# Kernel tuning notes

Hardware: AMD Instinct MI355X
Metric: run time of the kernel (lower is better)

The kernel has to match this reference:

```python
import jax, jax.numpy as jnp
import numpy as np

WINDOW_SIZE = 2
SOFTMAX_TEMP = 0.01
WIDTH = 320
EPS = 1e-12  # F.normalize default eps


def _l2norm(x, axis):
    n = jnp.sqrt(jnp.sum(x * x, axis=axis, keepdims=True))
    return x / jnp.maximum(n, EPS)


def setup_inputs() -> dict:
    key = jax.random.key(0)
    k1, k2, k3, k4 = jax.random.split(key, 4)
    BW, C, N, S = 4, 256, 1024, 1
    return {
        "keypoint_scores": jax.random.uniform(k1, (BW, S, N), dtype=jnp.float32),
        "keypoint_desc": jax.random.normal(k2, (BW, C, N), dtype=jnp.float32),
        "desc_dense": jax.random.normal(k3, (BW, C, WIDTH, WIDTH), dtype=jnp.float32),
        "keypoint_coords": jax.random.uniform(k4, (BW, N, 2), dtype=jnp.float32),
    }


def reference(keypoint_scores, keypoint_desc, desc_dense, keypoint_coords):
    BW, C, N = keypoint_desc.shape
    B = BW // WINDOW_SIZE
    P = B * (WINDOW_SIZE - 1)  # number of (src, tgt) pairs

    # dense source pixel coordinates (u=col, v=row), matching torch meshgrid 'ij'
    idx = jnp.arange(WIDTH * WIDTH)
    coords = jnp.stack([(idx % WIDTH).astype(jnp.float32),
                        (idx // WIDTH).astype(jnp.float32)], axis=1)  # (HW, 2)

    # pair indexing: for window i, targets are i*w+1 .. i*w+w-1, source is i*w
    tgt_ids = jnp.array([i * WINDOW_SIZE + j for i in range(B)
                         for j in range(1, WINDOW_SIZE)], dtype=jnp.int32)
    src_ids = (tgt_ids // WINDOW_SIZE) * WINDOW_SIZE

    # normalized dense source descriptors: (B, C, HW)
    src_dense = desc_dense[::WINDOW_SIZE].reshape(B, C, -1)
    src_un = _l2norm(src_dense, axis=1)
    src_sel = src_un[tgt_ids // WINDOW_SIZE]  # (P, C, HW)

    # normalized target keypoint descriptors: (P, C, N)
    tgt_n = _l2norm(keypoint_desc[tgt_ids], axis=1)

    # QK^T over descriptor channel: (P, N, HW)
    match_vals = jnp.einsum('pcn,pcm->pnm', tgt_n, src_sel)
    soft = jax.nn.softmax(match_vals / SOFTMAX_TEMP, axis=2)

    # soft-argmax coordinates: (P, N, 2)
    pseudo_coords = jnp.einsum('pnm,md->pnd', soft, coords)

    match_weights = keypoint_scores[tgt_ids]  # (P, S, N)
    return pseudo_coords, match_weights, tgt_ids, src_ids
```

## Files before the change

kernel.cpp:

```cpp
#include <hip/hip_runtime.h>
#include <stdint.h>

#define HW_      102400
#define C_       256
#define N_       1024
#define P_       2
#define TILES_   1600
#define CHUNKS_  64
#define CHUNK_PX 1600
#define ITERS_   25
#define NB_      8
#define K2_      144.269504088896340f
#define MOFF_    (-72.134752044448170f)

typedef __attribute__((ext_vector_type(8))) short bf16x8;
typedef __attribute__((ext_vector_type(4))) float f32x4;

#define WS_TGT_OFF  0
#define WS_PAR_OFF  1048576
#define WS_PN_OFF   5242880

#define SWR(r) (((r) ^ ((r) >> 3)) & 7)

__device__ __forceinline__ uint32_t packbf(float a, float b) {
  uint32_t r;
  asm("v_cvt_pk_bf16_f32 %0, %1, %2" : "=v"(r) : "v"(a), "v"(b));
  return r;
}
__device__ __forceinline__ float fexp2(float x) {
  return __builtin_amdgcn_exp2f(x);
}
__device__ __forceinline__ void dma16(const uint32_t* g, uint32_t* l) {
  __builtin_amdgcn_global_load_lds(
      (const __attribute__((address_space(1))) uint32_t*)g,
      (__attribute__((address_space(3))) uint32_t*)l, 16, 0, 0);
}

__global__ __launch_bounds__(256)
void k_pre(const float* __restrict__ dense, const float* __restrict__ kdesc,
           const float* __restrict__ kscores, uint32_t* __restrict__ PN,
           uint16_t* __restrict__ tgt, float* __restrict__ out) {
  const int bid = blockIdx.x;
  if (bid < P_ * TILES_) {
    const int p = bid / TILES_, tile = bid % TILES_;
    const int r  = threadIdx.x & 63;
    const int cq = threadIdx.x >> 6;
    const float* src = dense + (size_t)(p * 2) * C_ * HW_ + (size_t)(cq * 64) * HW_
                     + tile * 64 + r;
    float v[64];
    #pragma unroll
    for (int c = 0; c < 64; ++c) v[c] = src[(size_t)c * HW_];
    float s0 = 0.f, s1 = 0.f, s2 = 0.f, s3 = 0.f;
    #pragma unroll
    for (int c = 0; c < 64; c += 4) {
      s0 = fmaf(v[c + 0], v[c + 0], s0);
      s1 = fmaf(v[c + 1], v[c + 1], s1);
      s2 = fmaf(v[c + 2], v[c + 2], s2);
      s3 = fmaf(v[c + 3], v[c + 3], s3);
    }
    __shared__ float part[4][64];
    __shared__ float sinv[64];
    part[cq][r] = (s0 + s1) + (s2 + s3);
    __syncthreads();
    if (threadIdx.x < 64) {
      const float s = part[0][threadIdx.x] + part[1][threadIdx.x]
                    + part[2][threadIdx.x] + part[3][threadIdx.x];
      sinv[threadIdx.x] = 1.f / fmaxf(sqrtf(s), 1e-12f);
    }
    __syncthreads();
    const float inv = sinv[r];
    const int s8 = SWR(r);
    uint32_t* dst = PN + ((size_t)(p * TILES_ + tile) << 13) + r * 128 + cq * 32;
    #pragma unroll
    for (int rg = 0; rg < 8; ++rg) {
      uint4 wv;
      wv.x = packbf(v[rg * 8 + 0] * inv, v[rg * 8 + 1] * inv);
      wv.y = packbf(v[rg * 8 + 2] * inv, v[rg * 8 + 3] * inv);
      wv.z = packbf(v[rg * 8 + 4] * inv, v[rg * 8 + 5] * inv);
      wv.w = packbf(v[rg * 8 + 6] * inv, v[rg * 8 + 7] * inv);
      *(uint4*)&dst[(rg ^ s8) << 2] = wv;
    }
  } else {
    const int t = (bid - P_ * TILES_) * 256 + threadIdx.x;
    const int p = t >> 10, n = t & 1023;
    const float* src = kdesc + (size_t)(p * 2 + 1) * C_ * N_ + n;
    float s = 0.f;
    #pragma unroll 16
    for (int c = 0; c < C_; ++c) { const float v = src[c * N_]; s = fmaf(v, v, s); }
    const float inv = 1.f / fmaxf(sqrtf(s), 1e-12f);
    uint32_t* dst = (uint32_t*)(tgt + (size_t)t * C_);
    #pragma unroll 4
    for (int c8 = 0; c8 < C_; c8 += 8) {
      uint4 wv;
      wv.x = packbf(src[(c8 + 0) * N_] * inv, src[(c8 + 1) * N_] * inv);
      wv.y = packbf(src[(c8 + 2) * N_] * inv, src[(c8 + 3) * N_] * inv);
      wv.z = packbf(src[(c8 + 4) * N_] * inv, src[(c8 + 5) * N_] * inv);
      wv.w = packbf(src[(c8 + 6) * N_] * inv, src[(c8 + 7) * N_] * inv);
      *(uint4*)&dst[c8 / 2] = wv;
    }
    out[4096 + t] = kscores[(p * 2 + 1) * N_ + n];
  }
}

__global__ __launch_bounds__(512, 3)
void k_main(const uint32_t* __restrict__ PN, const uint16_t* __restrict__ tgt,
            float4* __restrict__ partials) {
  __shared__ uint32_t lds[2 * 64 * 128];

  const int bid = blockIdx.x;
  const int xcd = bid & 7;
  const int rr  = bid >> 3;
  const int nb  = rr & 7;
  const int grp = xcd + 8 * (rr >> 3);
  const int p     = grp >> 6;
  const int chunk = grp & 63;

  const int t    = threadIdx.x;
  const int lane = t & 63;
  const int w    = t >> 6;
  const int l15  = lane & 15;
  const int g4   = lane >> 4;
  const int h    = w & 1;
  const int q    = w >> 1;

  bf16x8 Bf[2][8];
  const int nbase = nb * 128 + q * 32;
  #pragma unroll
  for (int j = 0; j < 2; ++j) {
    const uint16_t* tp = tgt + (size_t)(p * N_ + nbase + j * 16 + l15) * C_ + g4 * 8;
    #pragma unroll
    for (int k = 0; k < 8; ++k) Bf[j][k] = *(const bf16x8*)(tp + k * 32);
  }

  float stS[2], stU[2], stV[2];
  #pragma unroll
  for (int j = 0; j < 2; ++j) { stS[j] = 0.f; stU[j] = 0.f; stV[j] = 0.f; }

  const int row0  = h * 32 + l15;
  const int row1  = row0 + 16;
  const int sw0   = SWR(row0) << 2;
  const int sw1   = SWR(row1) << 2;
  const int base0 = row0 * 128;
  const int base1 = row1 * 128;
  const int lr0   = h * 32 + g4 * 4;

  const uint32_t* PNp = PN + ((size_t)(p * TILES_ + chunk * 25) << 13) + w * 1024 + lane * 4;

  #pragma unroll
  for (int jj = 0; jj < 4; ++jj) dma16(PNp + jj * 256, &lds[w * 1024 + jj * 256]);
  __syncthreads();

  int rbuf = 0;
  for (int iter = 0; iter < ITERS_; ++iter) {
    if (iter + 1 < ITERS_) {
      const uint32_t* s = PNp + ((size_t)(iter + 1) << 13);
      uint32_t* d = &lds[(rbuf ^ 1) * 8192 + w * 1024];
      #pragma unroll
      for (int jj = 0; jj < 4; ++jj) dma16(s + jj * 256, d + jj * 256);
    }

    const uint32_t* bufR = &lds[rbuf * 8192];
    f32x4 acc[2][2];
    #pragma unroll
    for (int j = 0; j < 2; ++j) {
      acc[j][0] = (f32x4){0.f, 0.f, 0.f, 0.f};
      acc[j][1] = (f32x4){0.f, 0.f, 0.f, 0.f};
    }
    #pragma unroll
    for (int k = 0; k < 8; ++k) {
      const int col = k * 16 + g4 * 4;
      bf16x8 a0 = *(const bf16x8*)&bufR[base0 + (col ^ sw0)];
      bf16x8 a1 = *(const bf16x8*)&bufR[base1 + (col ^ sw1)];
      acc[0][0] = __builtin_amdgcn_mfma_f32_16x16x32_bf16(a0, Bf[0][k], acc[0][0], 0, 0, 0);
      acc[0][1] = __builtin_amdgcn_mfma_f32_16x16x32_bf16(a1, Bf[0][k], acc[0][1], 0, 0, 0);
      acc[1][0] = __builtin_amdgcn_mfma_f32_16x16x32_bf16(a0, Bf[1][k], acc[1][0], 0, 0, 0);
      acc[1][1] = __builtin_amdgcn_mfma_f32_16x16x32_bf16(a1, Bf[1][k], acc[1][1], 0, 0, 0);
    }

    const int rb = iter * 64 + lr0;
    #pragma unroll
    for (int s = 0; s < 2; ++s) {
      #pragma unroll
      for (int e = 0; e < 4; ++e) {
        const int r  = rb + s * 16 + e;
        const int vl = (r * 6554) >> 21;
        const float vf = (float)(chunk * 5 + vl);
        const float uf = (float)(r - vl * 320);
        #pragma unroll
        for (int j = 0; j < 2; ++j) {
          const float ev = fexp2(fmaf(K2_, acc[j][s][e], MOFF_));
          stS[j] += ev;
          stU[j] = fmaf(ev, uf, stU[j]);
          stV[j] = fmaf(ev, vf, stV[j]);
        }
      }
    }

    __syncthreads();
    rbuf ^= 1;
  }

  #pragma unroll
  for (int j = 0; j < 2; ++j) {
    float S = stS[j], U = stU[j], V = stV[j];
    S += __shfl_xor(S, 16, 64); U += __shfl_xor(U, 16, 64); V += __shfl_xor(V, 16, 64);
    S += __shfl_xor(S, 32, 64); U += __shfl_xor(U, 32, 64); V += __shfl_xor(V, 32, 64);
    if (lane < 16) {
      const int n = nbase + j * 16 + l15;
      partials[((size_t)(p * CHUNKS_ + chunk) * 2 + h) * N_ + n] = make_float4(S, U, V, 0.f);
    }
  }
}

__global__ void k_final(const float4* __restrict__ partials, float* __restrict__ out) {
  const int t = blockIdx.x * blockDim.x + threadIdx.x;
  const int p = t >> 10, n = t & 1023;
  float S = 0.f, U = 0.f, V = 0.f;
  #pragma unroll 4
  for (int s = 0; s < 2 * CHUNKS_; ++s) {
    const float4 v = partials[((size_t)p * 2 * CHUNKS_ + s) * N_ + n];
    S += v.x; U += v.y; V += v.z;
  }
  out[(size_t)(p * N_ + n) * 2 + 0] = U / S;
  out[(size_t)(p * N_ + n) * 2 + 1] = V / S;
  if (t < 4) {
    const float ids[4] = {1.f, 3.f, 0.f, 2.f};
    out[6144 + t] = ids[t];
  }
}

extern "C" void kernel_launch(void* const* d_in, const int* in_sizes, int n_in,
                              void* d_out, int out_size, void* d_ws, size_t ws_size,
                              hipStream_t stream) {
  const float* kscores = (const float*)d_in[0];
  const float* kdesc   = (const float*)d_in[1];
  const float* dense   = (const float*)d_in[2];
  float* out = (float*)d_out;

  char* ws = (char*)d_ws;
  uint16_t* tgt = (uint16_t*)(ws + WS_TGT_OFF);
  float4*   par = (float4*)(ws + WS_PAR_OFF);
  uint32_t* PN  = (uint32_t*)(ws + WS_PN_OFF);

  k_pre<<<P_ * TILES_ + (P_ * N_) / 256, 256, 0, stream>>>(dense, kdesc, kscores, PN, tgt, out);
  k_main<<<P_ * NB_ * CHUNKS_, 512, 0, stream>>>(PN, tgt, par);
  k_final<<<(P_ * N_) / 256, 256, 0, stream>>>(par, out);
}
```

Measured before the change: 219.8 us.

## Widen main blocks to 1024 threads, stage pre-normalize stores through LDS

```diff
diff --git a/kernel.cpp b/kernel.cpp
--- a/kernel.cpp
+++ b/kernel.cpp
@@ -6,10 +6,9 @@
 #define N_       1024
 #define P_       2
 #define TILES_   1600
-#define CHUNKS_  64
-#define CHUNK_PX 1600
-#define ITERS_   25
-#define NB_      8
+#define CHUNKS_  32
+#define ITERS_   50
+#define NB_      4
 #define K2_      144.269504088896340f
 #define MOFF_    (-72.134752044448170f)
 
@@ -17,8 +16,8 @@
 typedef __attribute__((ext_vector_type(4))) float f32x4;
 
 #define WS_TGT_OFF  0
-#define WS_PAR_OFF  1048576
-#define WS_PN_OFF   5242880
+#define WS_PAR_OFF  (1u << 20)
+#define WS_PN_OFF   (4u << 20)
 
 #define SWR(r) (((r) ^ ((r) >> 3)) & 7)
 
@@ -40,53 +39,69 @@
 void k_pre(const float* __restrict__ dense, const float* __restrict__ kdesc,
            const float* __restrict__ kscores, uint32_t* __restrict__ PN,
            uint16_t* __restrict__ tgt, float* __restrict__ out) {
+  __shared__ float part[16][64];
+  __shared__ float sinv[64];
+  __shared__ uint32_t T[8192];
   const int bid = blockIdx.x;
   if (bid < P_ * TILES_) {
     const int p = bid / TILES_, tile = bid % TILES_;
-    const int r  = threadIdx.x & 63;
-    const int cq = threadIdx.x >> 6;
-    const float* src = dense + (size_t)(p * 2) * C_ * HW_ + (size_t)(cq * 64) * HW_
-                     + tile * 64 + r;
-    float v[64];
-    #pragma unroll
-    for (int c = 0; c < 64; ++c) v[c] = src[(size_t)c * HW_];
-    float s0 = 0.f, s1 = 0.f, s2 = 0.f, s3 = 0.f;
-    #pragma unroll
-    for (int c = 0; c < 64; c += 4) {
-      s0 = fmaf(v[c + 0], v[c + 0], s0);
-      s1 = fmaf(v[c + 1], v[c + 1], s1);
-      s2 = fmaf(v[c + 2], v[c + 2], s2);
-      s3 = fmaf(v[c + 3], v[c + 3], s3);
-    }
-    __shared__ float part[4][64];
-    __shared__ float sinv[64];
-    part[cq][r] = (s0 + s1) + (s2 + s3);
-    __syncthreads();
-    if (threadIdx.x < 64) {
-      const float s = part[0][threadIdx.x] + part[1][threadIdx.x]
-                    + part[2][threadIdx.x] + part[3][threadIdx.x];
-      sinv[threadIdx.x] = 1.f / fmaxf(sqrtf(s), 1e-12f);
-    }
-    __syncthreads();
-    const float inv = sinv[r];
-    const int s8 = SWR(r);
-    uint32_t* dst = PN + ((size_t)(p * TILES_ + tile) << 13) + r * 128 + cq * 32;
-    #pragma unroll
-    for (int rg = 0; rg < 8; ++rg) {
-      uint4 wv;
-      wv.x = packbf(v[rg * 8 + 0] * inv, v[rg * 8 + 1] * inv);
-      wv.y = packbf(v[rg * 8 + 2] * inv, v[rg * 8 + 3] * inv);
-      wv.z = packbf(v[rg * 8 + 4] * inv, v[rg * 8 + 5] * inv);
-      wv.w = packbf(v[rg * 8 + 6] * inv, v[rg * 8 + 7] * inv);
-      *(uint4*)&dst[(rg ^ s8) << 2] = wv;
-    }
+    const int t   = threadIdx.x;
+    const int px4 = (t & 15) * 4;
+    const int cg  = t >> 4;
+    const float* src = dense + (size_t)(p * 2) * C_ * HW_ + (size_t)(cg * 16) * HW_
+                     + tile * 64 + px4;
+    float v[16][4];
+    #pragma unroll
+    for (int cc = 0; cc < 16; ++cc) {
+      const float4 q = *(const float4*)(src + (size_t)cc * HW_);
+      v[cc][0] = q.x; v[cc][1] = q.y; v[cc][2] = q.z; v[cc][3] = q.w;
+    }
+    float ps[4] = {0.f, 0.f, 0.f, 0.f};
+    #pragma unroll
+    for (int cc = 0; cc < 16; ++cc) {
+      #pragma unroll
+      for (int i = 0; i < 4; ++i) ps[i] = fmaf(v[cc][i], v[cc][i], ps[i]);
+    }
+    #pragma unroll
+    for (int i = 0; i < 4; ++i) part[cg][px4 + i] = ps[i];
+    __syncthreads();
+    if (t < 64) {
+      float s = 0.f;
+      #pragma unroll
+      for (int g = 0; g < 16; ++g) s += part[g][t];
+      sinv[t] = 1.f / fmaxf(sqrtf(s), 1e-12f);
+    }
+    __syncthreads();
+    #pragma unroll
+    for (int i = 0; i < 4; ++i) {
+      const int r  = px4 + i;
+      const float iv = sinv[r];
+      const int s8 = SWR(r);
+      uint32_t* dst = &T[r * 128];
+      uint4 A, B;
+      A.x = packbf(v[0][i] * iv,  v[1][i] * iv);
+      A.y = packbf(v[2][i] * iv,  v[3][i] * iv);
+      A.z = packbf(v[4][i] * iv,  v[5][i] * iv);
+      A.w = packbf(v[6][i] * iv,  v[7][i] * iv);
+      B.x = packbf(v[8][i] * iv,  v[9][i] * iv);
+      B.y = packbf(v[10][i] * iv, v[11][i] * iv);
+      B.z = packbf(v[12][i] * iv, v[13][i] * iv);
+      B.w = packbf(v[14][i] * iv, v[15][i] * iv);
+      *(uint4*)&dst[((2 * cg + 0) ^ s8) * 4] = A;
+      *(uint4*)&dst[((2 * cg + 1) ^ s8) * 4] = B;
+    }
+    __syncthreads();
+    uint32_t* dstg = PN + ((size_t)(p * TILES_ + tile) << 13) + t * 32;
+    #pragma unroll
+    for (int k = 0; k < 8; ++k)
+      *(uint4*)&dstg[k * 4] = *(const uint4*)&T[t * 32 + k * 4];
   } else {
     const int t = (bid - P_ * TILES_) * 256 + threadIdx.x;
     const int p = t >> 10, n = t & 1023;
     const float* src = kdesc + (size_t)(p * 2 + 1) * C_ * N_ + n;
     float s = 0.f;
     #pragma unroll 16
-    for (int c = 0; c < C_; ++c) { const float v = src[c * N_]; s = fmaf(v, v, s); }
+    for (int c = 0; c < C_; ++c) { const float v2 = src[c * N_]; s = fmaf(v2, v2, s); }
     const float inv = 1.f / fmaxf(sqrtf(s), 1e-12f);
     uint32_t* dst = (uint32_t*)(tgt + (size_t)t * C_);
     #pragma unroll 4
@@ -102,18 +117,18 @@
   }
 }
 
-__global__ __launch_bounds__(512, 3)
+__global__ __launch_bounds__(1024, 4)
 void k_main(const uint32_t* __restrict__ PN, const uint16_t* __restrict__ tgt,
             float4* __restrict__ partials) {
-  __shared__ uint32_t lds[2 * 64 * 128];
+  __shared__ uint32_t lds[2 * 8192];
 
   const int bid = blockIdx.x;
   const int xcd = bid & 7;
   const int rr  = bid >> 3;
-  const int nb  = rr & 7;
-  const int grp = xcd + 8 * (rr >> 3);
-  const int p     = grp >> 6;
-  const int chunk = grp & 63;
+  const int nb  = rr & 3;
+  const int grp = xcd + 8 * (rr >> 2);
+  const int p     = grp >> 5;
+  const int chunk = grp & 31;
 
   const int t    = threadIdx.x;
   const int lane = t & 63;
@@ -124,7 +139,7 @@
   const int q    = w >> 1;
 
   bf16x8 Bf[2][8];
-  const int nbase = nb * 128 + q * 32;
+  const int nbase = nb * 256 + q * 32;
   #pragma unroll
   for (int j = 0; j < 2; ++j) {
     const uint16_t* tp = tgt + (size_t)(p * N_ + nbase + j * 16 + l15) * C_ + g4 * 8;
@@ -137,35 +152,42 @@
   for (int j = 0; j < 2; ++j) { stS[j] = 0.f; stU[j] = 0.f; stV[j] = 0.f; }
 
   const int row0  = h * 32 + l15;
-  const int row1  = row0 + 16;
   const int sw0   = SWR(row0) << 2;
-  const int sw1   = SWR(row1) << 2;
+  const int sw1   = sw0 ^ 8;
   const int base0 = row0 * 128;
-  const int base1 = row1 * 128;
+  const int base1 = base0 + 16 * 128;
   const int lr0   = h * 32 + g4 * 4;
 
-  const uint32_t* PNp = PN + ((size_t)(p * TILES_ + chunk * 25) << 13) + w * 1024 + lane * 4;
-
-  #pragma unroll
-  for (int jj = 0; jj < 4; ++jj) dma16(PNp + jj * 256, &lds[w * 1024 + jj * 256]);
+  float offf[2][4];
+  #pragma unroll
+  for (int s = 0; s < 2; ++s)
+    #pragma unroll
+    for (int e = 0; e < 4; ++e) offf[s][e] = (float)(lr0 + s * 16 + e);
+
+  const uint32_t* PNp = PN + ((size_t)(p * TILES_ + chunk * ITERS_) << 13) + w * 512 + lane * 4;
+  uint32_t* ldsw0 = &lds[w * 512];
+
+  dma16(PNp, ldsw0);
+  dma16(PNp + 256, ldsw0 + 256);
   __syncthreads();
 
-  int rbuf = 0;
+  float u0f = 0.f, v0f = (float)(chunk * 10);
   for (int iter = 0; iter < ITERS_; ++iter) {
     if (iter + 1 < ITERS_) {
       const uint32_t* s = PNp + ((size_t)(iter + 1) << 13);
-      uint32_t* d = &lds[(rbuf ^ 1) * 8192 + w * 1024];
-      #pragma unroll
-      for (int jj = 0; jj < 4; ++jj) dma16(s + jj * 256, d + jj * 256);
-    }
-
-    const uint32_t* bufR = &lds[rbuf * 8192];
+      uint32_t* d = ldsw0 + ((iter & 1) ^ 1) * 8192;
+      dma16(s, d);
+      dma16(s + 256, d + 256);
+    }
+
+    const uint32_t* bufR = &lds[(iter & 1) * 8192];
     f32x4 acc[2][2];
     #pragma unroll
     for (int j = 0; j < 2; ++j) {
       acc[j][0] = (f32x4){0.f, 0.f, 0.f, 0.f};
       acc[j][1] = (f32x4){0.f, 0.f, 0.f, 0.f};
     }
+    __builtin_amdgcn_s_setprio(1);
     #pragma unroll
     for (int k = 0; k < 8; ++k) {
       const int col = k * 16 + g4 * 4;
@@ -176,28 +198,28 @@
       acc[1][0] = __builtin_amdgcn_mfma_f32_16x16x32_bf16(a0, Bf[1][k], acc[1][0], 0, 0, 0);
       acc[1][1] = __builtin_amdgcn_mfma_f32_16x16x32_bf16(a1, Bf[1][k], acc[1][1], 0, 0, 0);
     }
-
-    const int rb = iter * 64 + lr0;
-    #pragma unroll
-    for (int s = 0; s < 2; ++s) {
+    __builtin_amdgcn_s_setprio(0);
+
+    #pragma unroll
+    for (int j = 0; j < 2; ++j) {
+      float tS = 0.f, tU = 0.f;
       #pragma unroll
-      for (int e = 0; e < 4; ++e) {
-        const int r  = rb + s * 16 + e;
-        const int vl = (r * 6554) >> 21;
-        const float vf = (float)(chunk * 5 + vl);
-        const float uf = (float)(r - vl * 320);
+      for (int s = 0; s < 2; ++s) {
         #pragma unroll
-        for (int j = 0; j < 2; ++j) {
+        for (int e = 0; e < 4; ++e) {
           const float ev = fexp2(fmaf(K2_, acc[j][s][e], MOFF_));
-          stS[j] += ev;
-          stU[j] = fmaf(ev, uf, stU[j]);
-          stV[j] = fmaf(ev, vf, stV[j]);
+          tS += ev;
+          tU = fmaf(ev, offf[s][e], tU);
         }
       }
-    }
-
-    __syncthreads();
-    rbuf ^= 1;
+      stS[j] += tS;
+      stU[j] += fmaf(u0f, tS, tU);
+      stV[j] = fmaf(v0f, tS, stV[j]);
+    }
+    u0f += 64.f;
+    if (u0f > 290.f) { u0f = 0.f; v0f += 1.f; }
+
+    __syncthreads();
   }
 
   #pragma unroll
@@ -243,6 +265,6 @@
   uint32_t* PN  = (uint32_t*)(ws + WS_PN_OFF);
 
   k_pre<<<P_ * TILES_ + (P_ * N_) / 256, 256, 0, stream>>>(dense, kdesc, kscores, PN, tgt, out);
-  k_main<<<P_ * NB_ * CHUNKS_, 512, 0, stream>>>(PN, tgt, par);
+  k_main<<<P_ * NB_ * CHUNKS_, 1024, 0, stream>>>(PN, tgt, par);
   k_final<<<(P_ * N_) / 256, 256, 0, stream>>>(par, out);
 }
```

After: 189.2 us. -13.9%, faster.
